# Optimization experiments

Hardware: AMD Instinct MI355X
Metric: run time of the kernel (lower is better)

## Reference

```python
import jax, jax.numpy as jnp
import numpy as np

LEAKY_ALPHA = 0.2

def setup_inputs() -> dict:
    key = jax.random.key(0)
    kA, kH, kW, k1, k2 = jax.random.split(key, 5)
    B, N, F_in, D = 8, 2048, 256, 128
    return {
        "A": jax.random.normal(kA, (B, N, N), dtype=jnp.float32),
        "H": jax.random.normal(kH, (B, N, F_in), dtype=jnp.float32),
        "W": jax.random.normal(kW, (F_in, D), dtype=jnp.float32) * 0.05,
        "a_1": jax.random.normal(k1, (D, 1), dtype=jnp.float32) * 0.05,
        "a_2": jax.random.normal(k2, (D, 1), dtype=jnp.float32) * 0.05,
    }

def reference(A, H, W, a_1, a_2):
    # H_: [B, N, D] node projections
    H_ = jnp.einsum('bnf,fd->bnd', H, W)
    # additive attention logits: f1[b,i] + f2[b,j] -> [B, N, N]
    f1 = H_ @ a_1            # [B, N, 1]
    f2 = H_ @ a_2            # [B, N, 1]
    e = jax.nn.leaky_relu(f1 + jnp.swapaxes(f2, 1, 2), negative_slope=LEAKY_ALPHA)
    # NOTE: original multiplies logits by the binary adjacency (not -inf masking)
    mask = (A > 0.0).astype(jnp.float32)
    alpha = jax.nn.softmax(e * mask, axis=-1)   # [B, N, N]
    H_next = jnp.matmul(alpha, H_)              # [B, N, D]
    return H_next
```

## Files before the change

### kernel.cpp

```cpp
#include <hip/hip_runtime.h>


#define LEAKY 0.2f
constexpr int Bb = 8, Nn = 2048, FIN = 256, Dd = 128;
constexpr int NROW = Bb * Nn;
constexpr int RS = 132;

typedef __attribute__((ext_vector_type(8))) short short8;
typedef __attribute__((ext_vector_type(4))) float float4v;

__device__ __forceinline__ unsigned short f2bf(float f) {
    union { float f; unsigned int i; } v; v.f = f;
    return (unsigned short)((v.i + 0x8000u) >> 16);
}

__device__ __forceinline__ void stage_read(const float* __restrict__ base, int rstride,
                                           int tid, float4* st) {
    const int row = tid >> 4, c16 = tid & 15;
    const float* p = base + (size_t)row * rstride + c16 * 4;
    #pragma unroll
    for (int k = 0; k < 4; ++k) st[k] = *(const float4*)(p + 64 * k);
}
__device__ __forceinline__ void stage_write(float* __restrict__ As, int tid, const float4* st) {
    const int row = tid >> 4, c16 = tid & 15, sw = row & 7;
    float* dst = As + row * 256;
    #pragma unroll
    for (int k = 0; k < 4; ++k) {
        const int col = 4 * (c16 + 16 * k);
        dst[(col + 0) ^ sw] = st[k].x;
        dst[(col + 1) ^ sw] = st[k].y;
        dst[(col + 2) ^ sw] = st[k].z;
        dst[(col + 3) ^ sw] = st[k].w;
    }
}

__global__ __launch_bounds__(256) void prep_wf(const float* __restrict__ W,
                                               unsigned short* __restrict__ Wf) {
    int idx = blockIdx.x * 256 + threadIdx.x;
    int k = idx >> 7, d = idx & 127;
    Wf[(size_t)((k >> 3) * 128 + d) * 8 + (k & 7)] = f2bf(W[idx]);
}

__global__ __launch_bounds__(256) void proj_kernel(
    const float* __restrict__ Hg,
    const unsigned short* __restrict__ Wf,
    const float* __restrict__ a1, const float* __restrict__ a2,
    unsigned short* __restrict__ Hbt2,
    float* __restrict__ f1g, float* __restrict__ f2g) {
    __shared__ float Rbuf[4 * 16 * RS];
    __shared__ float Hs[4096];

    const int tid = threadIdx.x;
    const int w = tid >> 6, lane = tid & 63, q = lane >> 4, m = lane & 15;
    const int row0 = blockIdx.x * 16;

    float4 st[4];
    stage_read(Hg + (size_t)row0 * FIN, FIN, tid, st);
    stage_write(Hs, tid, st);
    __syncthreads();

    float4v acc[8] = {};
    const float* arow = Hs + m * 256;
    const int sw = m & 7;
    #pragma unroll
    for (int c = 0; c < 2; ++c) {
        const int cb = w * 64 + 32 * c + 8 * q;
        union { short8 v; unsigned short us[8]; } Af;
        #pragma unroll
        for (int j = 0; j < 8; ++j) Af.us[j] = f2bf(arow[cb + (j ^ sw)]);
        #pragma unroll
        for (int t = 0; t < 8; ++t) {
            const short8 bfr = *(const short8*)(Wf + (size_t)((8 * w + 4 * c + q) * 128 + 16 * t + m) * 8);
            acc[t] = __builtin_amdgcn_mfma_f32_16x16x32_bf16(Af.v, bfr, acc[t], 0, 0, 0);
        }
    }
    #pragma unroll
    for (int t = 0; t < 8; ++t)
        #pragma unroll
        for (int rg = 0; rg < 4; ++rg)
            Rbuf[w * 16 * RS + (4 * q + rg) * RS + 16 * t + m] = acc[t][rg];
    __syncthreads();

    const int row = tid >> 4, c4 = tid & 15;
    float o[8];
    #pragma unroll
    for (int half = 0; half < 2; ++half) {
        const int col = 64 * half + 4 * c4;
        const float* rb = Rbuf + row * RS + col;
        float4 s0 = *(const float4*)(rb);
        float4 s1 = *(const float4*)(rb + 16 * RS);
        float4 s2 = *(const float4*)(rb + 32 * RS);
        float4 s3 = *(const float4*)(rb + 48 * RS);
        o[4 * half + 0] = s0.x + s1.x + s2.x + s3.x;
        o[4 * half + 1] = s0.y + s1.y + s2.y + s3.y;
        o[4 * half + 2] = s0.z + s1.z + s2.z + s3.z;
        o[4 * half + 3] = s0.w + s1.w + s2.w + s3.w;
    }
    {
        float4 A1a = *(const float4*)(a1 + 4 * c4), A1b = *(const float4*)(a1 + 64 + 4 * c4);
        float4 A2a = *(const float4*)(a2 + 4 * c4), A2b = *(const float4*)(a2 + 64 + 4 * c4);
        float p1 = o[0]*A1a.x + o[1]*A1a.y + o[2]*A1a.z + o[3]*A1a.w
                 + o[4]*A1b.x + o[5]*A1b.y + o[6]*A1b.z + o[7]*A1b.w;
        float p2 = o[0]*A2a.x + o[1]*A2a.y + o[2]*A2a.z + o[3]*A2a.w
                 + o[4]*A2b.x + o[5]*A2b.y + o[6]*A2b.z + o[7]*A2b.w;
        #pragma unroll
        for (int off = 1; off <= 8; off <<= 1) {
            p1 += __shfl_xor(p1, off, 16);
            p2 += __shfl_xor(p2, off, 16);
        }
        if (c4 == 0) { f1g[row0 + row] = p1; f2g[row0 + row] = p2; }
    }
    *(float4*)(Rbuf + row * RS + 4 * c4)      = make_float4(o[0], o[1], o[2], o[3]);
    *(float4*)(Rbuf + row * RS + 64 + 4 * c4) = make_float4(o[4], o[5], o[6], o[7]);
    __syncthreads();
    const int d = tid >> 1, h = tid & 1;
    union { uint4 v; unsigned short us[8]; } oP;
    #pragma unroll
    for (int r = 0; r < 8; ++r) oP.us[r] = f2bf(Rbuf[(8 * h + r) * RS + d]);
    *(uint4*)(Hbt2 + (size_t)((2 * blockIdx.x + h) * 128 + d) * 8) = oP.v;
}

__global__ __launch_bounds__(256) void attn_kernel(
    const float* __restrict__ Ag,
    const unsigned short* __restrict__ Hbt2,
    const float* __restrict__ f1g, const float* __restrict__ f2g,
    float* __restrict__ Og) {
    __shared__ float smem[8448];
    __shared__ float f2s[2][256];
    __shared__ float Lbuf[4][16];

    const int tid = threadIdx.x;
    const int w = tid >> 6, lane = tid & 63, q = lane >> 4, m = lane & 15;
    const int b = blockIdx.y, i0 = blockIdx.x * 16;
    const size_t bRow = (size_t)b * Nn;

    const float fi = f1g[bRow + i0 + m];
    const float* Abase = Ag + (bRow + i0) * (size_t)Nn;
    const float* f2p = f2g + bRow;
    const unsigned short* Bb2 = Hbt2 + bRow * 128;
    const int jw = w * 64;

    float4v acc[8] = {};
    float lsum = 0.f;
    float4 st[4], fst;

    stage_read(Abase, Nn, tid, st);
    if (tid < 64) fst = *(const float4*)(f2p + tid * 4);
    stage_write(smem, tid, st);
    if (tid < 64) *(float4*)(&f2s[0][tid * 4]) = fst;

    for (int ch = 0; ch < 8; ++ch) {
        __syncthreads();
        const int jt = ch * 256;
        const float* As = smem + (ch & 1) * 4096;
        const float* f2c = &f2s[ch & 1][0];
        const unsigned short* bg = Bb2 + (size_t)((jt + jw) >> 3) * 1024;
        short8 bf[16];
        #pragma unroll
        for (int t = 0; t < 8; ++t) {
            bf[2 * t]     = *(const short8*)(bg + ((size_t)(q    ) * 128 + 16 * t + m) * 8);
            bf[2 * t + 1] = *(const short8*)(bg + ((size_t)(q + 4) * 128 + 16 * t + m) * 8);
        }
        __builtin_amdgcn_sched_barrier(0);
        if (ch < 7) {
            stage_read(Abase + jt + 256, Nn, tid, st);
            if (tid < 64) fst = *(const float4*)(f2p + jt + 256 + tid * 4);
        }
        __builtin_amdgcn_sched_barrier(0);
        const float* arow = As + m * 256;
        const int sw = m & 7;
        short8 pa[2];
        #pragma unroll
        for (int c = 0; c < 2; ++c) {
            const int cb = jw + 32 * c + 8 * q;
            union { short8 v; unsigned short us[8]; } P;
            #pragma unroll
            for (int j = 0; j < 8; ++j) {
                const float a = arow[cb + (j ^ sw)];
                const float s = fi + f2c[cb + j];
                float e = fmaxf(s, LEAKY * s);
                e = fminf(e, 30.f);
                const float p = (a > 0.f) ? __expf(e) : 1.0f;
                P.us[j] = f2bf(p);
                lsum += p;
            }
            pa[c] = P.v;
        }
        #pragma unroll
        for (int t = 0; t < 8; ++t) {
            acc[t] = __builtin_amdgcn_mfma_f32_16x16x32_bf16(pa[0], bf[2 * t],     acc[t], 0, 0, 0);
            acc[t] = __builtin_amdgcn_mfma_f32_16x16x32_bf16(pa[1], bf[2 * t + 1], acc[t], 0, 0, 0);
        }
        if (ch < 7) {
            stage_write(smem + ((ch + 1) & 1) * 4096, tid, st);
            if (tid < 64) *(float4*)(&f2s[(ch + 1) & 1][tid * 4]) = fst;
        }
    }

    __syncthreads();
    lsum += __shfl_xor(lsum, 16, 64);
    lsum += __shfl_xor(lsum, 32, 64);
    if (lane < 16) Lbuf[w][lane] = lsum;
    float* Rbuf = smem;
    #pragma unroll
    for (int t = 0; t < 8; ++t)
        #pragma unroll
        for (int rg = 0; rg < 4; ++rg)
            Rbuf[w * 16 * RS + (4 * q + rg) * RS + 16 * t + m] = acc[t][rg];
    __syncthreads();

    const int row = tid >> 4, c4 = tid & 15;
    float l = Lbuf[0][row] + Lbuf[1][row] + Lbuf[2][row] + Lbuf[3][row];
    float rl = 1.0f / l;
    float* orow = Og + (bRow + i0 + row) * (size_t)Dd;
    #pragma unroll
    for (int half = 0; half < 2; ++half) {
        const int col = 64 * half + 4 * c4;
        const float* rb = Rbuf + row * RS + col;
        float4 s0 = *(const float4*)(rb);
        float4 s1 = *(const float4*)(rb + 16 * RS);
        float4 s2 = *(const float4*)(rb + 32 * RS);
        float4 s3 = *(const float4*)(rb + 48 * RS);
        float4 o;
        o.x = (s0.x + s1.x + s2.x + s3.x) * rl;
        o.y = (s0.y + s1.y + s2.y + s3.y) * rl;
        o.z = (s0.z + s1.z + s2.z + s3.z) * rl;
        o.w = (s0.w + s1.w + s2.w + s3.w) * rl;
        *(float4*)(orow + col) = o;
    }
}

extern "C" void kernel_launch(void* const* d_in, const int* in_sizes, int n_in,
                              void* d_out, int out_size, void* d_ws, size_t ws_size,
                              hipStream_t stream) {
    const float* A  = (const float*)d_in[0];
    const float* H  = (const float*)d_in[1];
    const float* W  = (const float*)d_in[2];
    const float* a1 = (const float*)d_in[3];
    const float* a2 = (const float*)d_in[4];
    float* out = (float*)d_out;

    unsigned short* Wf   = (unsigned short*)d_ws;
    unsigned short* Hbt2 = Wf + FIN * Dd;
    float* f1 = (float*)(Hbt2 + (size_t)Dd * NROW);
    float* f2 = f1 + NROW;

    prep_wf<<<dim3(FIN * Dd / 256), 256, 0, stream>>>(W, Wf);
    proj_kernel<<<dim3(NROW / 16), 256, 0, stream>>>(H, Wf, a1, a2, Hbt2, f1, f2);
    attn_kernel<<<dim3(Nn / 16, Bb), 256, 0, stream>>>(A, Hbt2, f1, f2, out);
}
```

Baseline: 223.2 us.

## Load adjacency straight to registers per wave and drop LDS staging and barriers

The attention kernel no longer stages A and f2 tiles through double-buffered shared memory with a barrier each chunk. Each wave now owns a contiguous 512-column slice, prefetches A values and f2 into registers one step ahead, and broadcasts f2 with lane shuffles. The exponent becomes a raw v_exp_f32 (base 2), which works because f1 and f2 are pre-scaled by log2(e). The clamp at 30 is dropped. The row sum is computed on the matrix units by an MFMA against a vector of ones, and probabilities are packed with v_cvt_pk_bf16_f32. This removes LDS traffic, per-chunk synchronization and VALU reduction work, but drops overflow protection and makes the global access pattern less coalesced.

```diff
diff --git a/kernel.cpp b/kernel.cpp
--- a/kernel.cpp
+++ b/kernel.cpp
@@ -5,6 +5,7 @@
 constexpr int Bb = 8, Nn = 2048, FIN = 256, Dd = 128;
 constexpr int NROW = Bb * Nn;
 constexpr int RS = 132;
+constexpr float LOG2E = 1.44269504088896f;
 
 typedef __attribute__((ext_vector_type(8))) short short8;
 typedef __attribute__((ext_vector_type(4))) float float4v;
@@ -108,7 +109,7 @@
             p1 += __shfl_xor(p1, off, 16);
             p2 += __shfl_xor(p2, off, 16);
         }
-        if (c4 == 0) { f1g[row0 + row] = p1; f2g[row0 + row] = p2; }
+        if (c4 == 0) { f1g[row0 + row] = p1 * LOG2E; f2g[row0 + row] = p2 * LOG2E; }
     }
     *(float4*)(Rbuf + row * RS + 4 * c4)      = make_float4(o[0], o[1], o[2], o[3]);
     *(float4*)(Rbuf + row * RS + 64 + 4 * c4) = make_float4(o[4], o[5], o[6], o[7]);
@@ -125,9 +126,7 @@
     const unsigned short* __restrict__ Hbt2,
     const float* __restrict__ f1g, const float* __restrict__ f2g,
     float* __restrict__ Og) {
-    __shared__ float smem[8448];
-    __shared__ float f2s[2][256];
-    __shared__ float Lbuf[4][16];
+    __shared__ float Rbuf[4 * 16 * RS];
 
     const int tid = threadIdx.x;
     const int w = tid >> 6, lane = tid & 63, q = lane >> 4, m = lane & 15;
@@ -135,26 +134,32 @@
     const size_t bRow = (size_t)b * Nn;
 
     const float fi = f1g[bRow + i0 + m];
-    const float* Abase = Ag + (bRow + i0) * (size_t)Nn;
-    const float* f2p = f2g + bRow;
-    const unsigned short* Bb2 = Hbt2 + bRow * 128;
-    const int jw = w * 64;
+    const float* Arow = Ag + (bRow + i0 + m) * (size_t)Nn + 512 * w;
+    const float* f2w  = f2g + bRow + 512 * w;
+    const unsigned short* Hb = Hbt2 + bRow * 128;
+    const int g0w = 64 * w;
+
+    short8 ones;
+    #pragma unroll
+    for (int k = 0; k < 8; ++k) ones[k] = (short)0x3F80;
 
     float4v acc[8] = {};
-    float lsum = 0.f;
-    float4 st[4], fst;
-
-    stage_read(Abase, Nn, tid, st);
-    if (tid < 64) fst = *(const float4*)(f2p + tid * 4);
-    stage_write(smem, tid, st);
-    if (tid < 64) *(float4*)(&f2s[0][tid * 4]) = fst;
-
-    for (int ch = 0; ch < 8; ++ch) {
-        __syncthreads();
-        const int jt = ch * 256;
-        const float* As = smem + (ch & 1) * 4096;
-        const float* f2c = &f2s[ch & 1][0];
-        const unsigned short* bg = Bb2 + (size_t)((jt + jw) >> 3) * 1024;
+    float4v accl = {};
+
+    float4 av[2][4];
+    float f2r[2];
+
+    #pragma unroll
+    for (int c = 0; c < 2; ++c) {
+        av[0][2 * c]     = *(const float4*)(Arow + 32 * c + 8 * q);
+        av[0][2 * c + 1] = *(const float4*)(Arow + 32 * c + 8 * q + 4);
+    }
+    f2r[0] = f2w[lane];
+
+    #pragma unroll
+    for (int s = 0; s < 8; ++s) {
+        const int p = s & 1;
+        const unsigned short* bg = Hb + (size_t)(g0w + 8 * s) * 1024;
         short8 bf[16];
         #pragma unroll
         for (int t = 0; t < 8; ++t) {
@@ -162,27 +167,33 @@
             bf[2 * t + 1] = *(const short8*)(bg + ((size_t)(q + 4) * 128 + 16 * t + m) * 8);
         }
         __builtin_amdgcn_sched_barrier(0);
-        if (ch < 7) {
-            stage_read(Abase + jt + 256, Nn, tid, st);
-            if (tid < 64) fst = *(const float4*)(f2p + jt + 256 + tid * 4);
+        if (s < 7) {
+            #pragma unroll
+            for (int c = 0; c < 2; ++c) {
+                av[p ^ 1][2 * c]     = *(const float4*)(Arow + 64 * (s + 1) + 32 * c + 8 * q);
+                av[p ^ 1][2 * c + 1] = *(const float4*)(Arow + 64 * (s + 1) + 32 * c + 8 * q + 4);
+            }
+            f2r[p ^ 1] = f2w[64 * (s + 1) + lane];
         }
         __builtin_amdgcn_sched_barrier(0);
-        const float* arow = As + m * 256;
-        const int sw = m & 7;
         short8 pa[2];
         #pragma unroll
         for (int c = 0; c < 2; ++c) {
-            const int cb = jw + 32 * c + 8 * q;
-            union { short8 v; unsigned short us[8]; } P;
+            union { short8 v; unsigned int u[4]; } P;
             #pragma unroll
-            for (int j = 0; j < 8; ++j) {
-                const float a = arow[cb + (j ^ sw)];
-                const float s = fi + f2c[cb + j];
-                float e = fmaxf(s, LEAKY * s);
-                e = fminf(e, 30.f);
-                const float p = (a > 0.f) ? __expf(e) : 1.0f;
-                P.us[j] = f2bf(p);
-                lsum += p;
+            for (int k = 0; k < 4; ++k) {
+                float pv[2];
+                #pragma unroll
+                for (int hh = 0; hh < 2; ++hh) {
+                    const int j = 2 * k + hh;
+                    const float a  = ((const float*)&av[p][2 * c + (j >> 2)])[j & 3];
+                    const float s2 = fi + __shfl(f2r[p], 32 * c + 8 * q + j, 64);
+                    const float t2 = fmaxf(s2, LEAKY * s2);
+                    float e;
+                    asm("v_exp_f32 %0, %1" : "=v"(e) : "v"(t2));
+                    pv[hh] = (a > 0.f) ? e : 1.0f;
+                }
+                asm("v_cvt_pk_bf16_f32 %0, %1, %2" : "=v"(P.u[k]) : "v"(pv[0]), "v"(pv[1]));
             }
             pa[c] = P.v;
         }
@@ -191,27 +202,26 @@
             acc[t] = __builtin_amdgcn_mfma_f32_16x16x32_bf16(pa[0], bf[2 * t],     acc[t], 0, 0, 0);
             acc[t] = __builtin_amdgcn_mfma_f32_16x16x32_bf16(pa[1], bf[2 * t + 1], acc[t], 0, 0, 0);
         }
-        if (ch < 7) {
-            stage_write(smem + ((ch + 1) & 1) * 4096, tid, st);
-            if (tid < 64) *(float4*)(&f2s[(ch + 1) & 1][tid * 4]) = fst;
-        }
-    }
-
-    __syncthreads();
-    lsum += __shfl_xor(lsum, 16, 64);
-    lsum += __shfl_xor(lsum, 32, 64);
-    if (lane < 16) Lbuf[w][lane] = lsum;
-    float* Rbuf = smem;
+        accl = __builtin_amdgcn_mfma_f32_16x16x32_bf16(pa[0], ones, accl, 0, 0, 0);
+        accl = __builtin_amdgcn_mfma_f32_16x16x32_bf16(pa[1], ones, accl, 0, 0, 0);
+    }
+
     #pragma unroll
     for (int t = 0; t < 8; ++t)
         #pragma unroll
         for (int rg = 0; rg < 4; ++rg)
             Rbuf[w * 16 * RS + (4 * q + rg) * RS + 16 * t + m] = acc[t][rg];
+    if (m == 0) {
+        #pragma unroll
+        for (int rg = 0; rg < 4; ++rg)
+            Rbuf[w * 16 * RS + (4 * q + rg) * RS + 128] = accl[rg];
+    }
     __syncthreads();
 
     const int row = tid >> 4, c4 = tid & 15;
-    float l = Lbuf[0][row] + Lbuf[1][row] + Lbuf[2][row] + Lbuf[3][row];
-    float rl = 1.0f / l;
+    const float l = Rbuf[row * RS + 128] + Rbuf[16 * RS + row * RS + 128]
+                  + Rbuf[32 * RS + row * RS + 128] + Rbuf[48 * RS + row * RS + 128];
+    const float rl = 1.0f / l;
     float* orow = Og + (bRow + i0 + row) * (size_t)Dd;
     #pragma unroll
     for (int half = 0; half < 2; ++half) {
```

Result: no change. 227.2 us (+1.8%).
